# Performance work log

Measured on AMD Instinct MI355X. Metric: run time of the kernel, lower is better.

Reference implementation:

```python
import jax, jax.numpy as jnp
import numpy as np

B, S, H = 2, 2048, 4096
NH, HD = 16, 256          # num heads, head size (H = NH * HD)
RD = 64                   # rotary_dim (GPT-J style partial rotary)
ROPE_BASE = 10000.0
SCALE = HD ** -0.5


def setup_inputs() -> dict:
    key = jax.random.key(0)
    k1, k2, k3 = jax.random.split(key, 3)
    hidden_states = jax.random.normal(k1, (B, S, H), dtype=jnp.float32) * 0.02
    position_ids = jnp.broadcast_to(jnp.arange(S, dtype=jnp.int32), (B, S))
    w_qkv = jax.random.normal(k2, (H, 3 * H), dtype=jnp.float32) * 0.02
    w_out = jax.random.normal(k3, (H, H), dtype=jnp.float32) * 0.02
    return {"hidden_states": hidden_states, "position_ids": position_ids,
            "w_qkv": w_qkv, "w_out": w_out}


def _rope_gptj(x, positions):
    # x: [B, S, NH, HD]; GPT-J interleaved (non-neox) RoPE on first RD dims
    inv_freq = 1.0 / (ROPE_BASE ** (jnp.arange(0, RD, 2, dtype=jnp.float32) / RD))
    freqs = positions.astype(jnp.float32)[..., None] * inv_freq   # [B,S,RD/2]
    cos = jnp.cos(freqs)[:, :, None, :]                            # [B,S,1,RD/2]
    sin = jnp.sin(freqs)[:, :, None, :]
    x_rot, x_pass = x[..., :RD], x[..., RD:]
    x1, x2 = x_rot[..., 0::2], x_rot[..., 1::2]                    # interleaved pairs
    o1 = x1 * cos - x2 * sin
    o2 = x2 * cos + x1 * sin
    rot = jnp.stack([o1, o2], axis=-1).reshape(x_rot.shape)        # re-interleave
    return jnp.concatenate([rot, x_pass], axis=-1)


def reference(hidden_states, position_ids, w_qkv, w_out):
    # fused QKV projection; note Moss splits as q, v, k
    qkv = jnp.einsum('bsh,hf->bsf', hidden_states, w_qkv)
    q, v, k = jnp.split(qkv, 3, axis=-1)
    q = q.reshape(B, S, NH, HD)
    k = k.reshape(B, S, NH, HD)
    v = v.reshape(B, S, NH, HD)
    q = _rope_gptj(q, position_ids)
    k = _rope_gptj(k, position_ids)
    # causal scaled dot-product attention
    scores = jnp.einsum('bqhd,bkhd->bhqk', q, k) * SCALE           # [B,NH,S,S]
    causal = jnp.tril(jnp.ones((S, S), dtype=bool))
    scores = jnp.where(causal, scores, jnp.finfo(scores.dtype).min)
    probs = jax.nn.softmax(scores, axis=-1)
    attn = jnp.einsum('bhqk,bkhd->bqhd', probs, v).reshape(B, S, H)
    return jnp.einsum('bsh,ho->bso', attn, w_out)
```

## Files before the change

kernel.cpp:

```cpp
#include <hip/hip_runtime.h>
#include <hip/hip_bf16.h>
#include <cmath>

#define B_ 2
#define S_ 2048
#define H_ 4096
#define NH_ 16
#define HD_ 256
#define RD_ 64
#define F3_ 12288
#define TOK_ (B_*S_)

static constexpr float SCALE_ = 0.0625f;

typedef __bf16 bf16;
typedef bf16 bf16x8 __attribute__((ext_vector_type(8)));
typedef bf16 bf16x4 __attribute__((ext_vector_type(4)));
typedef float f32x4 __attribute__((ext_vector_type(4)));

union BU2 { unsigned int u; bf16 h[2]; };

__global__ void k_tcvt(const float* __restrict__ in, bf16* __restrict__ out, int R, int C) {
  __shared__ float tile[32][33];
  int c0 = blockIdx.x * 32, r0 = blockIdx.y * 32;
  int x = threadIdx.x, y = threadIdx.y;
#pragma unroll
  for (int k = 0; k < 4; ++k)
    tile[y + 8 * k][x] = in[(size_t)(r0 + y + 8 * k) * C + c0 + x];
  __syncthreads();
#pragma unroll
  for (int k = 0; k < 4; ++k)
    out[(size_t)(c0 + y + 8 * k) * R + r0 + x] = (bf16)tile[x][y + 8 * k];
}

__global__ void k_rope_table(float* __restrict__ cosT, float* __restrict__ sinT) {
  int pos = blockIdx.x, j = threadIdx.x;
  float invf = (float)pow(10000.0, -2.0 * (double)j / 64.0);
  float ang = (float)pos * invf;
  cosT[pos * 32 + j] = cosf(ang);
  sinT[pos * 32 + j] = sinf(ang);
}

__global__ void k_rope_reorder(const bf16* __restrict__ qkv, const int* __restrict__ pid,
                               const float* __restrict__ cosT, const float* __restrict__ sinT,
                               bf16* __restrict__ Qo, bf16* __restrict__ Ko) {
  int tok = blockIdx.x;
  int b = tok >> 11, s = tok & (S_ - 1);
  int t = threadIdx.x;
  int hh = t >> 7, tt = t & 127;
  int pos = pid[tok];
  int d = tt * 2;
  float c = 1.f, sn = 0.f;
  if (tt < 32) { c = cosT[pos * 32 + tt]; sn = sinT[pos * 32 + tt]; }
#pragma unroll
  for (int hs = 0; hs < 8; ++hs) {
    int h = hs * 2 + hh;
    size_t iq = (size_t)tok * F3_ + h * HD_ + d;
    size_t oo = ((size_t)(b * NH_ + h) * S_ + s) * HD_ + d;
    BU2 q; q.u = *(const unsigned int*)(qkv + iq);
    BU2 k; k.u = *(const unsigned int*)(qkv + iq + 2 * H_);
    BU2 qo, ko;
    if (tt < 32) {
      float q1 = (float)q.h[0], q2 = (float)q.h[1];
      float k1 = (float)k.h[0], k2 = (float)k.h[1];
      qo.h[0] = (bf16)(q1 * c - q2 * sn); qo.h[1] = (bf16)(q2 * c + q1 * sn);
      ko.h[0] = (bf16)(k1 * c - k2 * sn); ko.h[1] = (bf16)(k2 * c + k1 * sn);
    } else { qo = q; ko = k; }
    *(unsigned int*)(Qo + oo) = qo.u;
    *(unsigned int*)(Ko + oo) = ko.u;
  }
}

__global__ void k_vtrans(const bf16* __restrict__ qkv, bf16* __restrict__ VT) {
  __shared__ float tile[64][129];
  int bid = blockIdx.x;
  int st = bid & 31, bh = bid >> 5;
  int b = bh >> 4, h = bh & 15;
  int t = threadIdx.x;
  for (int half = 0; half < 2; ++half) {
#pragma unroll
    for (int r = 0; r < 16; ++r) {
      int i = r * 4 + (t >> 6);
      int d = (t & 63) * 2;
      int s = st * 64 + i;
      size_t idx = (size_t)(b * S_ + s) * F3_ + H_ + h * HD_ + half * 128 + d;
      BU2 v; v.u = *(const unsigned int*)(qkv + idx);
      tile[i][d] = (float)v.h[0];
      tile[i][d + 1] = (float)v.h[1];
    }
    __syncthreads();
    int i = t & 63, dg = t >> 6;
    size_t ob = ((size_t)bh * HD_ + half * 128) * S_ + st * 64 + i;
#pragma unroll
    for (int dd = 0; dd < 32; ++dd) {
      int dcol = dd * 4 + dg;
      VT[ob + (size_t)dcol * S_] = (bf16)tile[i][dcol];
    }
    __syncthreads();
  }
}

template <bool A_F32, bool OUT_F32>
__global__ __launch_bounds__(256, 3)
void k_gemm(const void* __restrict__ Av, const bf16* __restrict__ BT,
            void* __restrict__ Cv, int Mm, int Nn, int Kk, int gx) {
  __shared__ bf16 As[2][128 * 40];
  __shared__ bf16 Bs[2][128 * 40];

  int nwg = gridDim.x;
  int bid = blockIdx.x;
  int cpx = nwg >> 3;
  int wg = (bid & 7) * cpx + (bid >> 3);
  int bx = wg % gx, by = wg / gx;
  int n0 = bx * 128, m0 = by * 128;

  int tid = threadIdx.x;
  int lane = tid & 63, wv = tid >> 6;
  int wr = wv >> 1, wc = wv & 1;

  const f32x4 Z4 = {0.f, 0.f, 0.f, 0.f};
  f32x4 acc[4][4];
#pragma unroll
  for (int i = 0; i < 4; ++i)
#pragma unroll
    for (int j = 0; j < 4; ++j) acc[i][j] = Z4;

  const int NT = Kk >> 5;

  float4 areg[4];
  bf16x8 areg16[2];
  bf16x8 breg[2];

  auto loadT = [&](int t) {
    int k0 = t * 32;
    if (A_F32) {
      const float* A = (const float*)Av;
#pragma unroll
      for (int r = 0; r < 4; ++r) {
        int row = r * 32 + (tid >> 3);
        areg[r] = *(const float4*)(A + (size_t)(m0 + row) * Kk + k0 + (tid & 7) * 4);
      }
    } else {
      const bf16* A = (const bf16*)Av;
#pragma unroll
      for (int r = 0; r < 2; ++r) {
        int row = r * 64 + (tid >> 2);
        areg16[r] = *(const bf16x8*)(A + (size_t)(m0 + row) * Kk + k0 + (tid & 3) * 8);
      }
    }
#pragma unroll
    for (int r = 0; r < 2; ++r) {
      int row = r * 64 + (tid >> 2);
      breg[r] = *(const bf16x8*)(BT + (size_t)(n0 + row) * Kk + k0 + (tid & 3) * 8);
    }
  };
  auto writeLds = [&](int buf) {
    if (A_F32) {
#pragma unroll
      for (int r = 0; r < 4; ++r) {
        int row = r * 32 + (tid >> 3);
        bf16x4 v;
        v[0] = (bf16)areg[r].x; v[1] = (bf16)areg[r].y;
        v[2] = (bf16)areg[r].z; v[3] = (bf16)areg[r].w;
        *(bf16x4*)&As[buf][row * 40 + (tid & 7) * 4] = v;
      }
    } else {
#pragma unroll
      for (int r = 0; r < 2; ++r) {
        int row = r * 64 + (tid >> 2);
        *(bf16x8*)&As[buf][row * 40 + (tid & 3) * 8] = areg16[r];
      }
    }
#pragma unroll
    for (int r = 0; r < 2; ++r) {
      int row = r * 64 + (tid >> 2);
      *(bf16x8*)&Bs[buf][row * 40 + (tid & 3) * 8] = breg[r];
    }
  };

  loadT(0);
  writeLds(0);
  __syncthreads();
  int cur = 0;
  for (int t = 0; t < NT; ++t) {
    if (t + 1 < NT) loadT(t + 1);
    bf16x8 af[4], bfr[4];
    int ko = (lane >> 4) * 8;
#pragma unroll
    for (int mt = 0; mt < 4; ++mt)
      af[mt] = *(const bf16x8*)&As[cur][(wr * 64 + mt * 16 + (lane & 15)) * 40 + ko];
#pragma unroll
    for (int nt = 0; nt < 4; ++nt)
      bfr[nt] = *(const bf16x8*)&Bs[cur][(wc * 64 + nt * 16 + (lane & 15)) * 40 + ko];
#pragma unroll
    for (int mt = 0; mt < 4; ++mt)
#pragma unroll
      for (int nt = 0; nt < 4; ++nt)
        acc[mt][nt] = __builtin_amdgcn_mfma_f32_16x16x32_bf16(af[mt], bfr[nt], acc[mt][nt], 0, 0, 0);
    if (t + 1 < NT) writeLds(cur ^ 1);
    __syncthreads();
    cur ^= 1;
  }

#pragma unroll
  for (int mt = 0; mt < 4; ++mt)
#pragma unroll
    for (int nt = 0; nt < 4; ++nt)
#pragma unroll
      for (int r = 0; r < 4; ++r) {
        int m = m0 + wr * 64 + mt * 16 + (lane >> 4) * 4 + r;
        int n = n0 + wc * 64 + nt * 16 + (lane & 15);
        if (OUT_F32)
          ((float*)Cv)[(size_t)m * Nn + n] = acc[mt][nt][r];
        else
          ((bf16*)Cv)[(size_t)m * Nn + n] = (bf16)acc[mt][nt][r];
      }
}

__global__ __launch_bounds__(256, 2)
void k_attn(const bf16* __restrict__ Q, const bf16* __restrict__ K,
            const bf16* __restrict__ VT, bf16* __restrict__ O) {
  __shared__ bf16 Ks[64 * 256];
  __shared__ bf16 Vs[256 * 64];
  __shared__ bf16 Ps[4][16 * 80];

  int qt = blockIdx.x;
  int bh = blockIdx.y;
  int tid = threadIdx.x;
  int lane = tid & 63, wv = tid >> 6;

  int qrow = qt * 64 + wv * 16 + (lane & 15);
  const bf16* Qb = Q + ((size_t)bh * S_ + qrow) * HD_;
  bf16x8 qf[8];
#pragma unroll
  for (int dc = 0; dc < 8; ++dc)
    qf[dc] = *(const bf16x8*)(Qb + dc * 32 + (lane >> 4) * 8);

  const f32x4 Z4 = {0.f, 0.f, 0.f, 0.f};
  f32x4 o[16];
#pragma unroll
  for (int i = 0; i < 16; ++i) o[i] = Z4;
  float m_i[4], l_i[4];
#pragma unroll
  for (int r = 0; r < 4; ++r) { m_i[r] = -INFINITY; l_i[r] = 0.f; }

  const bf16* Kb = K + (size_t)bh * S_ * HD_;
  const bf16* Vb = VT + (size_t)bh * HD_ * S_;

  for (int t = 0; t <= qt; ++t) {
    int kv0 = t * 64;
    {
      int i0 = tid >> 5;
      int doff = (tid & 31) * 8;
#pragma unroll
      for (int it = 0; it < 8; ++it) {
        int row = it * 8 + i0;
        bf16x8 g = *(const bf16x8*)(Kb + (size_t)(kv0 + row) * HD_ + doff);
        int el = (row * 256 + doff) ^ ((row & 7) << 3);
        *(bf16x8*)&Ks[el] = g;
      }
      int d0 = tid >> 3;
      int koff = (tid & 7) * 8;
#pragma unroll
      for (int it = 0; it < 8; ++it) {
        int dr = it * 32 + d0;
        bf16x8 g = *(const bf16x8*)(Vb + (size_t)dr * S_ + kv0 + koff);
        int el = (dr * 64 + koff) ^ ((dr & 7) << 3);
        *(bf16x8*)&Vs[el] = g;
      }
    }
    __syncthreads();

    f32x4 sa[4];
#pragma unroll
    for (int nt = 0; nt < 4; ++nt) sa[nt] = Z4;
#pragma unroll
    for (int dc = 0; dc < 8; ++dc)
#pragma unroll
      for (int nt = 0; nt < 4; ++nt) {
        int kvr = nt * 16 + (lane & 15);
        int el = (kvr * 256 + dc * 32 + (lane >> 4) * 8) ^ ((kvr & 7) << 3);
        sa[nt] = __builtin_amdgcn_mfma_f32_16x16x32_bf16(qf[dc], *(const bf16x8*)&Ks[el], sa[nt], 0, 0, 0);
      }

    float p[4][4], mx[4];
    bool diag = (t == qt);
#pragma unroll
    for (int r = 0; r < 4; ++r) {
      float vmax = -INFINITY;
#pragma unroll
      for (int nt = 0; nt < 4; ++nt) {
        float v = sa[nt][r] * SCALE_;
        if (diag) {
          int q_abs = qt * 64 + wv * 16 + (lane >> 4) * 4 + r;
          int kv_abs = kv0 + nt * 16 + (lane & 15);
          if (kv_abs > q_abs) v = -1e30f;
        }
        p[nt][r] = v;
        vmax = fmaxf(vmax, v);
      }
      mx[r] = vmax;
    }
#pragma unroll
    for (int off = 1; off < 16; off <<= 1)
#pragma unroll
      for (int r = 0; r < 4; ++r) mx[r] = fmaxf(mx[r], __shfl_xor(mx[r], off));
    float sf[4], rs[4];
#pragma unroll
    for (int r = 0; r < 4; ++r) {
      float mnew = fmaxf(m_i[r], mx[r]);
      sf[r] = __expf(m_i[r] - mnew);
      float sum = 0.f;
#pragma unroll
      for (int nt = 0; nt < 4; ++nt) {
        p[nt][r] = __expf(p[nt][r] - mnew);
        sum += p[nt][r];
      }
      rs[r] = sum;
      m_i[r] = mnew;
    }
#pragma unroll
    for (int off = 1; off < 16; off <<= 1)
#pragma unroll
      for (int r = 0; r < 4; ++r) rs[r] += __shfl_xor(rs[r], off);
#pragma unroll
    for (int r = 0; r < 4; ++r) l_i[r] = l_i[r] * sf[r] + rs[r];
#pragma unroll
    for (int dt = 0; dt < 16; ++dt)
#pragma unroll
      for (int r = 0; r < 4; ++r) o[dt][r] *= sf[r];

#pragma unroll
    for (int nt = 0; nt < 4; ++nt)
#pragma unroll
      for (int r = 0; r < 4; ++r)
        Ps[wv][((lane >> 4) * 4 + r) * 80 + nt * 16 + (lane & 15)] = (bf16)p[nt][r];

#pragma unroll
    for (int kc = 0; kc < 2; ++kc) {
      bf16x8 pf = *(const bf16x8*)&Ps[wv][(lane & 15) * 80 + kc * 32 + (lane >> 4) * 8];
#pragma unroll
      for (int dt = 0; dt < 16; ++dt) {
        int drow = dt * 16 + (lane & 15);
        int el = (drow * 64 + kc * 32 + (lane >> 4) * 8) ^ ((drow & 7) << 3);
        o[dt] = __builtin_amdgcn_mfma_f32_16x16x32_bf16(pf, *(const bf16x8*)&Vs[el], o[dt], 0, 0, 0);
      }
    }
    __syncthreads();
  }

  int b = bh >> 4, h = bh & 15;
  float inv[4];
#pragma unroll
  for (int r = 0; r < 4; ++r) inv[r] = 1.0f / l_i[r];
#pragma unroll
  for (int dt = 0; dt < 16; ++dt)
#pragma unroll
    for (int r = 0; r < 4; ++r) {
      int q_abs = qt * 64 + wv * 16 + (lane >> 4) * 4 + r;
      O[((size_t)(b * S_ + q_abs)) * H_ + h * HD_ + dt * 16 + (lane & 15)] = (bf16)(o[dt][r] * inv[r]);
    }
}

extern "C" void kernel_launch(void* const* d_in, const int* in_sizes, int n_in,
                              void* d_out, int out_size, void* d_ws, size_t ws_size,
                              hipStream_t stream) {
  const float* hidden = (const float*)d_in[0];
  const int* pid = (const int*)d_in[1];
  const float* wqkv = (const float*)d_in[2];
  const float* wout = (const float*)d_in[3];
  float* outp = (float*)d_out;
  char* ws = (char*)d_ws;

  const size_t OFF_WQT = 0;
  const size_t OFF_WOT = OFF_WQT + (size_t)F3_ * H_ * 2;
  const size_t OFF_QKV = OFF_WOT + (size_t)H_ * H_ * 2;
  const size_t OFF_O = OFF_QKV;
  const size_t OFF_Q = OFF_QKV + (size_t)TOK_ * F3_ * 2;
  const size_t OFF_K = OFF_Q + (size_t)TOK_ * H_ * 2;
  const size_t OFF_VT = OFF_K + (size_t)TOK_ * H_ * 2;
  const size_t OFF_COS = OFF_VT + (size_t)TOK_ * H_ * 2;
  const size_t OFF_SIN = OFF_COS + (size_t)S_ * 32 * 4;
  const size_t TOTAL = OFF_SIN + (size_t)S_ * 32 * 4;
  if (ws_size < TOTAL) return;

  bf16* WqT = (bf16*)(ws + OFF_WQT);
  bf16* WoT = (bf16*)(ws + OFF_WOT);
  bf16* qkv = (bf16*)(ws + OFF_QKV);
  bf16* Obuf = (bf16*)(ws + OFF_O);
  bf16* Qb = (bf16*)(ws + OFF_Q);
  bf16* Kb = (bf16*)(ws + OFF_K);
  bf16* VTb = (bf16*)(ws + OFF_VT);
  float* cosT = (float*)(ws + OFF_COS);
  float* sinT = (float*)(ws + OFF_SIN);

  k_tcvt<<<dim3(F3_ / 32, H_ / 32), dim3(32, 8), 0, stream>>>(wqkv, WqT, H_, F3_);
  k_tcvt<<<dim3(H_ / 32, H_ / 32), dim3(32, 8), 0, stream>>>(wout, WoT, H_, H_);
  k_rope_table<<<dim3(S_), dim3(32), 0, stream>>>(cosT, sinT);
  k_gemm<true, false><<<dim3((F3_ / 128) * (TOK_ / 128)), dim3(256), 0, stream>>>(
      hidden, WqT, qkv, TOK_, F3_, H_, F3_ / 128);
  k_rope_reorder<<<dim3(TOK_), dim3(256), 0, stream>>>(qkv, pid, cosT, sinT, Qb, Kb);
  k_vtrans<<<dim3(B_ * NH_ * (S_ / 64)), dim3(256), 0, stream>>>(qkv, VTb);
  k_attn<<<dim3(S_ / 64, B_ * NH_), dim3(256), 0, stream>>>(Qb, Kb, VTb, Obuf);
  k_gemm<false, true><<<dim3((H_ / 128) * (TOK_ / 128)), dim3(256), 0, stream>>>(
      Obuf, WoT, outp, TOK_, H_, H_, H_ / 128);
}
```

Measured before the change: 1.664 ms.

## Replace GEMM with 256x256-tile direct-to-LDS pipelined MFMA kernel

Replaces the 128x128 register-staged GEMM with a 512-thread, 256x256-tile kernel. It loads tiles straight into LDS with global_load_lds, uses a swizzled layout, and interleaves loads with MFMA phases under manual waitcnt, barriers and setprio. The fp32 hidden states are first converted to bf16 by a separate kernel so both GEMMs take bf16 inputs, and the XCD-aware block remap now handles grids that do not divide evenly by 8. This aims to cut LDS traffic, register staging and load latency in the two projections, at the cost of an extra conversion pass, hard-coded K=4096 and fragile manual synchronisation.

```diff
diff --git a/kernel.cpp b/kernel.cpp
--- a/kernel.cpp
+++ b/kernel.cpp
@@ -19,6 +19,17 @@
 typedef float f32x4 __attribute__((ext_vector_type(4)));
 
 union BU2 { unsigned int u; bf16 h[2]; };
+
+__global__ void k_hcvt(const float* __restrict__ in, bf16* __restrict__ out, int n8) {
+  int i = blockIdx.x * 256 + threadIdx.x;
+  if (i >= n8) return;
+  const float4* p = (const float4*)in + (size_t)i * 2;
+  float4 a = p[0], b = p[1];
+  bf16x8 v;
+  v[0] = (bf16)a.x; v[1] = (bf16)a.y; v[2] = (bf16)a.z; v[3] = (bf16)a.w;
+  v[4] = (bf16)b.x; v[5] = (bf16)b.y; v[6] = (bf16)b.z; v[7] = (bf16)b.w;
+  ((bf16x8*)out)[i] = v;
+}
 
 __global__ void k_tcvt(const float* __restrict__ in, bf16* __restrict__ out, int R, int C) {
   __shared__ float tile[32][33];
@@ -100,120 +111,141 @@
   }
 }
 
-template <bool A_F32, bool OUT_F32>
-__global__ __launch_bounds__(256, 3)
-void k_gemm(const void* __restrict__ Av, const bf16* __restrict__ BT,
-            void* __restrict__ Cv, int Mm, int Nn, int Kk, int gx) {
-  __shared__ bf16 As[2][128 * 40];
-  __shared__ bf16 Bs[2][128 * 40];
+
+#define GK_ 4096
+
+#define STG(dst, half, src, row0, k0)                                                     \
+  do {                                                                                    \
+    const bf16* _s0 = (src) + (size_t)((row0) + (half) * 128 + sr0) * GK_ + (k0) + sc0;   \
+    const bf16* _s1 = (src) + (size_t)((row0) + (half) * 128 + sr1) * GK_ + (k0) + sc1;   \
+    __builtin_amdgcn_global_load_lds(                                                     \
+        (const __attribute__((address_space(1))) void*)_s0,                               \
+        (__attribute__((address_space(3))) void*)((char*)(dst) + (half) * 16384 + so0),   \
+        16, 0, 0);                                                                        \
+    __builtin_amdgcn_global_load_lds(                                                     \
+        (const __attribute__((address_space(1))) void*)_s1,                               \
+        (__attribute__((address_space(3))) void*)((char*)(dst) + (half) * 16384 + so1),   \
+        16, 0, 0);                                                                        \
+  } while (0)
+
+#define LDA(buf, mh)                                                                      \
+  _Pragma("unroll") for (int mt = 0; mt < 4; ++mt)                                        \
+  _Pragma("unroll") for (int kk = 0; kk < 2; ++kk)                                        \
+    aF[mt][kk] = *(const bf16x8*)((const char*)(buf) + aBase + ((mh)*4 + mt) * 2048 + kk * 64);
+
+#define LDB(dst, buf, nh)                                                                 \
+  _Pragma("unroll") for (int nt = 0; nt < 2; ++nt)                                        \
+  _Pragma("unroll") for (int kk = 0; kk < 2; ++kk)                                        \
+    dst[nt][kk] = *(const bf16x8*)((const char*)(buf) + bBase + ((nh)*2 + nt) * 2048 + kk * 64);
+
+#define MM(mh, nh, bfrag)                                                                 \
+  _Pragma("unroll") for (int mt = 0; mt < 4; ++mt)                                        \
+  _Pragma("unroll") for (int nt = 0; nt < 2; ++nt)                                        \
+  _Pragma("unroll") for (int kk = 0; kk < 2; ++kk)                                        \
+    acc[(mh)*4 + mt][(nh)*2 + nt] = __builtin_amdgcn_mfma_f32_16x16x32_bf16(              \
+        aF[mt][kk], bfrag[nt][kk], acc[(mh)*4 + mt][(nh)*2 + nt], 0, 0, 0);
+
+#define BAR __builtin_amdgcn_s_barrier()
+#define LGKM0 asm volatile("s_waitcnt lgkmcnt(0)" ::: "memory")
+#define VMW4 asm volatile("s_waitcnt vmcnt(4)" ::: "memory")
+#define VMW0 asm volatile("s_waitcnt vmcnt(0)" ::: "memory")
+#define PRIO1 __builtin_amdgcn_s_setprio(1)
+#define PRIO0 __builtin_amdgcn_s_setprio(0)
+
+template <bool OUT_F32>
+__global__ __launch_bounds__(512, 1)
+void k_gemm8(const bf16* __restrict__ A, const bf16* __restrict__ BT,
+             void* __restrict__ Cv, int Nn, int gx) {
+  __shared__ bf16 As0[256 * 64];
+  __shared__ bf16 As1[256 * 64];
+  __shared__ bf16 Bs0[256 * 64];
+  __shared__ bf16 Bs1[256 * 64];
 
   int nwg = gridDim.x;
   int bid = blockIdx.x;
-  int cpx = nwg >> 3;
-  int wg = (bid & 7) * cpx + (bid >> 3);
+  int q = nwg >> 3, r = nwg & 7;
+  int xcd = bid & 7, lid = bid >> 3;
+  int wg = (xcd < r ? xcd * (q + 1) : r * (q + 1) + (xcd - r) * q) + lid;
   int bx = wg % gx, by = wg / gx;
-  int n0 = bx * 128, m0 = by * 128;
+  int m0 = by * 256, n0 = bx * 256;
 
   int tid = threadIdx.x;
-  int lane = tid & 63, wv = tid >> 6;
-  int wr = wv >> 1, wc = wv & 1;
+  int lane = tid & 63, w = tid >> 6;
+  int wr = w >> 2, wc = w & 3;
+  int lrow = lane & 15, g = lane >> 4;
+  int sig = (lrow >> 2) & 1;
+  int cswz = (g * 16) ^ (sig << 5);
+  int aBase = (wr * 128 + lrow) * 128 + cswz;
+  int bBase = (wc * 64 + lrow) * 128 + cswz;
+
+  int ci0 = w * 64 + lane;
+  int ci1 = 512 + ci0;
+  int sr0 = ci0 >> 3, sr1 = ci1 >> 3;
+  int sc0 = ((ci0 & 7) ^ (((ci0 >> 5) & 1) << 1)) * 8;
+  int sc1 = ((ci1 & 7) ^ (((ci1 >> 5) & 1) << 1)) * 8;
+  int so0 = ci0 * 16, so1 = ci1 * 16;
+
+  STG(As0, 0, A, m0, 0);
+  STG(As0, 1, A, m0, 0);
+  STG(Bs0, 0, BT, n0, 0);
+  STG(Bs0, 1, BT, n0, 0);
+  STG(Bs1, 0, BT, n0, 64);
+  STG(Bs1, 1, BT, n0, 64);
 
   const f32x4 Z4 = {0.f, 0.f, 0.f, 0.f};
-  f32x4 acc[4][4];
-#pragma unroll
-  for (int i = 0; i < 4; ++i)
-#pragma unroll
-    for (int j = 0; j < 4; ++j) acc[i][j] = Z4;
-
-  const int NT = Kk >> 5;
-
-  float4 areg[4];
-  bf16x8 areg16[2];
-  bf16x8 breg[2];
-
-  auto loadT = [&](int t) {
-    int k0 = t * 32;
-    if (A_F32) {
-      const float* A = (const float*)Av;
-#pragma unroll
-      for (int r = 0; r < 4; ++r) {
-        int row = r * 32 + (tid >> 3);
-        areg[r] = *(const float4*)(A + (size_t)(m0 + row) * Kk + k0 + (tid & 7) * 4);
-      }
-    } else {
-      const bf16* A = (const bf16*)Av;
-#pragma unroll
-      for (int r = 0; r < 2; ++r) {
-        int row = r * 64 + (tid >> 2);
-        areg16[r] = *(const bf16x8*)(A + (size_t)(m0 + row) * Kk + k0 + (tid & 3) * 8);
-      }
-    }
-#pragma unroll
-    for (int r = 0; r < 2; ++r) {
-      int row = r * 64 + (tid >> 2);
-      breg[r] = *(const bf16x8*)(BT + (size_t)(n0 + row) * Kk + k0 + (tid & 3) * 8);
-    }
-  };
-  auto writeLds = [&](int buf) {
-    if (A_F32) {
-#pragma unroll
-      for (int r = 0; r < 4; ++r) {
-        int row = r * 32 + (tid >> 3);
-        bf16x4 v;
-        v[0] = (bf16)areg[r].x; v[1] = (bf16)areg[r].y;
-        v[2] = (bf16)areg[r].z; v[3] = (bf16)areg[r].w;
-        *(bf16x4*)&As[buf][row * 40 + (tid & 7) * 4] = v;
-      }
-    } else {
-#pragma unroll
-      for (int r = 0; r < 2; ++r) {
-        int row = r * 64 + (tid >> 2);
-        *(bf16x8*)&As[buf][row * 40 + (tid & 3) * 8] = areg16[r];
-      }
-    }
-#pragma unroll
-    for (int r = 0; r < 2; ++r) {
-      int row = r * 64 + (tid >> 2);
-      *(bf16x8*)&Bs[buf][row * 40 + (tid & 3) * 8] = breg[r];
-    }
-  };
-
-  loadT(0);
-  writeLds(0);
-  __syncthreads();
-  int cur = 0;
-  for (int t = 0; t < NT; ++t) {
-    if (t + 1 < NT) loadT(t + 1);
-    bf16x8 af[4], bfr[4];
-    int ko = (lane >> 4) * 8;
-#pragma unroll
-    for (int mt = 0; mt < 4; ++mt)
-      af[mt] = *(const bf16x8*)&As[cur][(wr * 64 + mt * 16 + (lane & 15)) * 40 + ko];
+  f32x4 acc[8][4];
+#pragma unroll
+  for (int i = 0; i < 8; ++i)
+#pragma unroll
+    for (int jj = 0; jj < 4; ++jj) acc[i][jj] = Z4;
+
+  bf16x8 aF[4][2], bFa[2][2], bFb[2][2];
+
+  VMW4;
+  BAR;
+
+  const int NIT = GK_ / 128;
+  for (int j = 0; j < NIT; ++j) {
+    bool last = (j == NIT - 1);
+    int kT1 = (2 * j + 1) * 64;
+    int kT2 = (2 * j + 2) * 64;
+    int kT3 = (2 * j + 3) * 64;
+    LDA(As0, 0); LDB(bFa, Bs0, 0);
+    STG(As1, 0, A, m0, kT1);
+    BAR; LGKM0; PRIO1; MM(0, 0, bFa); PRIO0; BAR;
+    LDB(bFb, Bs0, 1);
+    STG(As1, 1, A, m0, kT1);
+    BAR; LGKM0; PRIO1; MM(0, 1, bFb); PRIO0; BAR;
+    LDA(As0, 1);
+    if (!last) STG(Bs0, 0, BT, n0, kT2);
+    BAR; LGKM0; PRIO1; MM(1, 1, bFb); PRIO0; BAR;
+    if (!last) { STG(Bs0, 1, BT, n0, kT2); VMW4; } else { VMW0; }
+    BAR; PRIO1; MM(1, 0, bFa); PRIO0; BAR;
+    LDA(As1, 0); LDB(bFa, Bs1, 0);
+    if (!last) STG(As0, 0, A, m0, kT2);
+    BAR; LGKM0; PRIO1; MM(0, 0, bFa); PRIO0; BAR;
+    LDB(bFb, Bs1, 1);
+    if (!last) STG(As0, 1, A, m0, kT2);
+    BAR; LGKM0; PRIO1; MM(0, 1, bFb); PRIO0; BAR;
+    LDA(As1, 1);
+    if (!last) STG(Bs1, 0, BT, n0, kT3);
+    BAR; LGKM0; PRIO1; MM(1, 1, bFb); PRIO0; BAR;
+    if (!last) { STG(Bs1, 1, BT, n0, kT3); VMW4; }
+    BAR; PRIO1; MM(1, 0, bFa); PRIO0; BAR;
+  }
+
+#pragma unroll
+  for (int mt = 0; mt < 8; ++mt)
 #pragma unroll
     for (int nt = 0; nt < 4; ++nt)
-      bfr[nt] = *(const bf16x8*)&Bs[cur][(wc * 64 + nt * 16 + (lane & 15)) * 40 + ko];
-#pragma unroll
-    for (int mt = 0; mt < 4; ++mt)
-#pragma unroll
-      for (int nt = 0; nt < 4; ++nt)
-        acc[mt][nt] = __builtin_amdgcn_mfma_f32_16x16x32_bf16(af[mt], bfr[nt], acc[mt][nt], 0, 0, 0);
-    if (t + 1 < NT) writeLds(cur ^ 1);
-    __syncthreads();
-    cur ^= 1;
-  }
-
-#pragma unroll
-  for (int mt = 0; mt < 4; ++mt)
-#pragma unroll
-    for (int nt = 0; nt < 4; ++nt)
-#pragma unroll
-      for (int r = 0; r < 4; ++r) {
-        int m = m0 + wr * 64 + mt * 16 + (lane >> 4) * 4 + r;
-        int n = n0 + wc * 64 + nt * 16 + (lane & 15);
+#pragma unroll
+      for (int rr = 0; rr < 4; ++rr) {
+        int m = m0 + wr * 128 + mt * 16 + g * 4 + rr;
+        int n = n0 + wc * 64 + nt * 16 + lrow;
         if (OUT_F32)
-          ((float*)Cv)[(size_t)m * Nn + n] = acc[mt][nt][r];
+          ((float*)Cv)[(size_t)m * Nn + n] = acc[mt][nt][rr];
         else
-          ((bf16*)Cv)[(size_t)m * Nn + n] = (bf16)acc[mt][nt][r];
+          ((bf16*)Cv)[(size_t)m * Nn + n] = (bf16)acc[mt][nt][rr];
       }
 }
 
@@ -255,18 +287,18 @@
 #pragma unroll
       for (int it = 0; it < 8; ++it) {
         int row = it * 8 + i0;
-        bf16x8 g = *(const bf16x8*)(Kb + (size_t)(kv0 + row) * HD_ + doff);
+        bf16x8 gld = *(const bf16x8*)(Kb + (size_t)(kv0 + row) * HD_ + doff);
         int el = (row * 256 + doff) ^ ((row & 7) << 3);
-        *(bf16x8*)&Ks[el] = g;
+        *(bf16x8*)&Ks[el] = gld;
       }
       int d0 = tid >> 3;
       int koff = (tid & 7) * 8;
 #pragma unroll
       for (int it = 0; it < 8; ++it) {
         int dr = it * 32 + d0;
-        bf16x8 g = *(const bf16x8*)(Vb + (size_t)dr * S_ + kv0 + koff);
+        bf16x8 gld = *(const bf16x8*)(Vb + (size_t)dr * S_ + kv0 + koff);
         int el = (dr * 64 + koff) ^ ((dr & 7) << 3);
-        *(bf16x8*)&Vs[el] = g;
+        *(bf16x8*)&Vs[el] = gld;
       }
     }
     __syncthreads();
@@ -393,15 +425,17 @@
   bf16* VTb = (bf16*)(ws + OFF_VT);
   float* cosT = (float*)(ws + OFF_COS);
   float* sinT = (float*)(ws + OFF_SIN);
+  bf16* HB = (bf16*)(ws + OFF_Q);
 
   k_tcvt<<<dim3(F3_ / 32, H_ / 32), dim3(32, 8), 0, stream>>>(wqkv, WqT, H_, F3_);
   k_tcvt<<<dim3(H_ / 32, H_ / 32), dim3(32, 8), 0, stream>>>(wout, WoT, H_, H_);
   k_rope_table<<<dim3(S_), dim3(32), 0, stream>>>(cosT, sinT);
-  k_gemm<true, false><<<dim3((F3_ / 128) * (TOK_ / 128)), dim3(256), 0, stream>>>(
-      hidden, WqT, qkv, TOK_, F3_, H_, F3_ / 128);
+  k_hcvt<<<dim3(TOK_ * H_ / 8 / 256), dim3(256), 0, stream>>>(hidden, HB, TOK_ * H_ / 8);
+  k_gemm8<false><<<dim3((F3_ / 256) * (TOK_ / 256)), dim3(512), 0, stream>>>(
+      HB, WqT, qkv, F3_, F3_ / 256);
   k_rope_reorder<<<dim3(TOK_), dim3(256), 0, stream>>>(qkv, pid, cosT, sinT, Qb, Kb);
   k_vtrans<<<dim3(B_ * NH_ * (S_ / 64)), dim3(256), 0, stream>>>(qkv, VTb);
   k_attn<<<dim3(S_ / 64, B_ * NH_), dim3(256), 0, stream>>>(Qb, Kb, VTb, Obuf);
-  k_gemm<false, true><<<dim3((H_ / 128) * (TOK_ / 128)), dim3(256), 0, stream>>>(
-      Obuf, WoT, outp, TOK_, H_, H_, H_ / 128);
-}
+  k_gemm8<true><<<dim3((H_ / 256) * (TOK_ / 256)), dim3(512), 0, stream>>>(
+      Obuf, WoT, outp, H_, H_ / 256);
+}
```

Result: faster. 1.561 ms (-6.2%).
